# Kernel tuning notes

Hardware: AMD Instinct MI355X
Metric: run time of the kernel (lower is better)

## Reference

```python
import jax, jax.numpy as jnp
import numpy as np

NUM_HEADS = 16
ROPE_BASE = 10000.0


def _rope_cos_sin(seq_len, head_dim, dtype):
    # freqs for the half-dim; original caches cat(freqs, freqs) and then applies
    # the rotation per-half, which is equivalent to using the half-size tables.
    inv_freq = 1.0 / (ROPE_BASE ** (jnp.arange(0, head_dim, 2, dtype=jnp.float32) / head_dim))
    t = jnp.arange(seq_len, dtype=jnp.float32)
    freqs = jnp.einsum('i,j->ij', t, inv_freq)  # [S, hd/2]
    return jnp.cos(freqs).astype(dtype), jnp.sin(freqs).astype(dtype)


def _apply_rotary(x, cos, sin):
    # x: [B, H, S, hd]; cos/sin: [S, hd/2] broadcast over B, H
    half = x.shape[-1] // 2
    x1, x2 = x[..., :half], x[..., half:]
    return jnp.concatenate([x1 * cos - x2 * sin, x2 * cos + x1 * sin], axis=-1)


def setup_inputs() -> dict:
    key = jax.random.key(0)
    ks = jax.random.split(key, 5)
    D = 2048
    B, S = 2, 2048
    std = 1.0 / np.sqrt(D)
    return {
        'x': jax.random.normal(ks[0], (B, S, D), dtype=jnp.float32),
        'Wq': jax.random.normal(ks[1], (D, D), dtype=jnp.float32) * std,
        'Wk': jax.random.normal(ks[2], (D, D), dtype=jnp.float32) * std,
        'Wv': jax.random.normal(ks[3], (D, D), dtype=jnp.float32) * std,
        'Wo': jax.random.normal(ks[4], (D, D), dtype=jnp.float32) * std,
    }


def reference(x, Wq, Wk, Wv, Wo):
    B, S, D = x.shape
    H = NUM_HEADS
    hd = D // H
    scale = hd ** -0.5

    def proj(W):  # torch Linear: y = x @ W.T -> [B, H, S, hd]
        return (x @ W.T).reshape(B, S, H, hd).transpose(0, 2, 1, 3)

    q, k, v = proj(Wq), proj(Wk), proj(Wv)

    cos, sin = _rope_cos_sin(S, hd, x.dtype)
    q = _apply_rotary(q, cos, sin)
    k = _apply_rotary(k, cos, sin)

    scores = jnp.einsum('bhqd,bhkd->bhqk', q, k) * scale  # full O(S^2) scores
    attn = jax.nn.softmax(scores, axis=-1)
    out = jnp.einsum('bhqk,bhkd->bhqd', attn, v)
    out = out.transpose(0, 2, 1, 3).reshape(B, S, D)
    return out @ Wo.T
```

## Files before the change

kernel.cpp:

```cpp
#include <hip/hip_runtime.h>
#include <cstdint>

typedef __attribute__((ext_vector_type(8))) short bf16x8;
typedef __attribute__((ext_vector_type(4))) float f32x4;

__device__ inline unsigned short f2bf(float f) {
  uint32_t u = __float_as_uint(f);
  uint32_t lsb = (u >> 16) & 1u;
  u += 0x7fffu + lsb;
  return (unsigned short)(u >> 16);
}
__device__ inline float bf2f(unsigned short b) {
  return __uint_as_float(((uint32_t)b) << 16);
}

#define GLOAD16(gp, lp)                                                        \
  __builtin_amdgcn_global_load_lds(                                            \
      (const __attribute__((address_space(1))) void*)(gp),                     \
      (__attribute__((address_space(3))) void*)(lp), 16, 0, 0)

__global__ void cvt_f32_bf16(const float* __restrict__ in,
                             unsigned short* __restrict__ out, int n) {
  int i = (blockIdx.x * 256 + threadIdx.x) * 4;
  if (i >= n) return;
  float4 v = *(const float4*)(in + i);
  unsigned short o[4] = {f2bf(v.x), f2bf(v.y), f2bf(v.z), f2bf(v.w)};
  *(uint64_t*)(out + i) = *(const uint64_t*)o;
}

__global__ void rope_table_k(float* __restrict__ ctab, float* __restrict__ stab) {
  int i = blockIdx.x * 256 + threadIdx.x;
  int s = i >> 6, j = i & 63;
  float invf = expf(-(float)j * (9.210340371976184f / 64.0f));
  float ang = (float)s * invf;
  ctab[i] = cosf(ang);
  stab[i] = sinf(ang);
}

__global__ void rope_apply_k(unsigned short* __restrict__ qb,
                             unsigned short* __restrict__ kb,
                             const float* __restrict__ ctab,
                             const float* __restrict__ stab) {
  int row = blockIdx.x * 4 + (threadIdx.x >> 6);
  int t = threadIdx.x & 63;
  int s = row & 2047;
  int bh = (row >> 11) & 31;
  unsigned short* base = (row >> 16) ? kb : qb;
  unsigned short* p = base + ((size_t)bh * 2048 + s) * 128;
  float c = ctab[s * 64 + t], sn = stab[s * 64 + t];
  float x1 = bf2f(p[t]), x2 = bf2f(p[t + 64]);
  p[t] = f2bf(x1 * c - x2 * sn);
  p[t + 64] = f2bf(x2 * c + x1 * sn);
}

__global__ void transpose_v_k(const unsigned short* __restrict__ v,
                              unsigned short* __restrict__ vt) {
  __shared__ unsigned short tile[64][72];
  int bh = blockIdx.x, st = blockIdx.y, dt = blockIdx.z;
  const unsigned short* src = v + ((size_t)bh * 2048 + st * 64) * 128 + dt * 64;
  unsigned short* dst = vt + ((size_t)bh * 128 + dt * 64) * 2048 + st * 64;
  int t = threadIdx.x;
  int r = t >> 2, c0 = (t & 3) * 16;
  *(bf16x8*)&tile[r][c0] = *(const bf16x8*)(src + (size_t)r * 128 + c0);
  *(bf16x8*)&tile[r][c0 + 8] = *(const bf16x8*)(src + (size_t)r * 128 + c0 + 8);
  __syncthreads();
  unsigned short o[16];
#pragma unroll
  for (int i = 0; i < 16; i++) o[i] = tile[c0 + i][r];
  *(bf16x8*)(dst + (size_t)r * 2048 + c0) = *(const bf16x8*)&o[0];
  *(bf16x8*)(dst + (size_t)r * 2048 + c0 + 8) = *(const bf16x8*)&o[8];
}

template <int EPI>
__global__ __launch_bounds__(256, 2) void gemm_bt(
    const unsigned short* __restrict__ A, const unsigned short* __restrict__ Bm,
    float* __restrict__ Cf, unsigned short* __restrict__ q_out,
    unsigned short* __restrict__ k_out, unsigned short* __restrict__ v_out,
    int M, int N, int K) {
  __shared__ unsigned short sA[128 * 32];
  __shared__ unsigned short sB[128 * 32];
  const int t = threadIdx.x;
  const int w = t >> 6, l = t & 63;
  const int wr = w >> 1, wc = w & 1;
  const int bm = blockIdx.x * 128, bn = blockIdx.y * 128;
  const int lr = l & 15, lg = l >> 4;
  f32x4 acc[4][4] = {};

  const int srow = w * 16 + (l >> 2);
  const int sseg = (l & 3) * 8;
  const unsigned short* ga = A + (size_t)(bm + srow) * K + sseg;
  const unsigned short* gb = Bm + (size_t)(bn + srow) * K + sseg;
  unsigned short* lA = sA + w * 512 + l * 8;
  unsigned short* lB = sB + w * 512 + l * 8;

  for (int kt = 0; kt < K; kt += 32) {
    __syncthreads();
    GLOAD16(ga + kt, lA);
    GLOAD16(ga + kt + (size_t)64 * K, lA + 2048);
    GLOAD16(gb + kt, lB);
    GLOAD16(gb + kt + (size_t)64 * K, lB + 2048);
    __syncthreads();
    bf16x8 af[4], bfv[4];
#pragma unroll
    for (int m = 0; m < 4; m++)
      af[m] = *(const bf16x8*)(sA + (wr * 64 + m * 16 + lr) * 32 + lg * 8);
#pragma unroll
    for (int n = 0; n < 4; n++)
      bfv[n] = *(const bf16x8*)(sB + (wc * 64 + n * 16 + lr) * 32 + lg * 8);
#pragma unroll
    for (int m = 0; m < 4; m++)
#pragma unroll
      for (int n = 0; n < 4; n++)
        acc[m][n] = __builtin_amdgcn_mfma_f32_16x16x32_bf16(af[m], bfv[n],
                                                            acc[m][n], 0, 0, 0);
  }

#pragma unroll
  for (int m = 0; m < 4; m++) {
#pragma unroll
    for (int n = 0; n < 4; n++) {
      int gm0 = bm + wr * 64 + m * 16 + lg * 4;
      int gn = bn + wc * 64 + n * 16 + lr;
#pragma unroll
      for (int j = 0; j < 4; j++) {
        float v = acc[m][n][j];
        int gm = gm0 + j;
        if (EPI == 0) {
          Cf[(size_t)gm * N + gn] = v;
        } else {
          int which = gn >> 11, rem = gn & 2047;
          int h = rem >> 7, d = rem & 127;
          int b = gm >> 11, s = gm & 2047;
          unsigned short* dst = which == 0 ? q_out : (which == 1 ? k_out : v_out);
          dst[(((size_t)(b * 16 + h)) * 2048 + s) * 128 + d] = f2bf(v);
        }
      }
    }
  }
}

__global__ __launch_bounds__(256, 2) void attn_k(
    const unsigned short* __restrict__ Q, const unsigned short* __restrict__ K,
    const unsigned short* __restrict__ Vt, unsigned short* __restrict__ ctx) {
  __shared__ unsigned short sK[2][64 * 128];
  __shared__ unsigned short sV[2][128 * 64];
  __shared__ unsigned short sP[4][16 * 72];

  const int bh = blockIdx.x, qt = blockIdx.y;
  const int t = threadIdx.x;
  const int w = t >> 6, l = t & 63;
  const int lr = l & 15, lg = l >> 4;
  const int b = bh >> 4, h = bh & 15;
  const int q0 = qt * 64 + w * 16;
  const unsigned short* Qp = Q + ((size_t)bh * 2048 + q0) * 128;
  const unsigned short* Kbh = K + (size_t)bh * 2048 * 128;
  const unsigned short* Vbh = Vt + (size_t)bh * 128 * 2048;

  int gko[4], gvo[4];
#pragma unroll
  for (int i = 0; i < 4; i++) {
    int p = i * 256 + t;
    int rK = p >> 4, cK = p & 15;
    gko[i] = rK * 128 + ((cK ^ (rK & 7)) * 8);
    int rV = p >> 3, cV = p & 7;
    gvo[i] = rV * 2048 + ((cV ^ (rV & 7)) * 8);
  }

  bf16x8 qf[4];
#pragma unroll
  for (int ks = 0; ks < 4; ks++)
    qf[ks] = *(const bf16x8*)(Qp + lr * 128 + ks * 32 + lg * 8);

  f32x4 o[8];
#pragma unroll
  for (int i = 0; i < 8; i++) o[i] = (f32x4)0.0f;
  float m_r = -1e30f, l_r = 0.0f;
  const float kSc = 0.08838834764831845f * 1.4426950408889634f;
  char* pl = (char*)sP[w];

#define STAGE_KV(buf, kv)                                                      \
  do {                                                                         \
    _Pragma("unroll") for (int i = 0; i < 4; i++)                              \
        GLOAD16(Kbh + (size_t)(kv)*128 + gko[i],                               \
                sK[buf] + (i * 256 + t) * 8);                                  \
    _Pragma("unroll") for (int i = 0; i < 4; i++)                              \
        GLOAD16(Vbh + (size_t)(kv) + gvo[i], sV[buf] + (i * 256 + t) * 8);     \
  } while (0)

  STAGE_KV(0, 0);
  __syncthreads();

  for (int it = 0; it < 32; ++it) {
    const int cur = it & 1;
    if (it < 31) STAGE_KV(cur ^ 1, (it + 1) * 64);

    const char* kb = (const char*)sK[cur];
    const char* vbb = (const char*)sV[cur];

    f32x4 st[4];
#pragma unroll
    for (int mf = 0; mf < 4; mf++) {
      st[mf] = (f32x4)0.0f;
      const int rr = mf * 16 + lr;
      const int sw = (rr & 7) << 4;
#pragma unroll
      for (int ks = 0; ks < 4; ks++) {
        bf16x8 kf = *(const bf16x8*)(kb + rr * 256 + ((ks * 64 + lg * 16) ^ sw));
        st[mf] = __builtin_amdgcn_mfma_f32_16x16x32_bf16(kf, qf[ks], st[mf], 0, 0, 0);
      }
    }

    float sm[16];
    float tmax = -1e30f;
#pragma unroll
    for (int i = 0; i < 16; i++) {
      sm[i] = st[i >> 2][i & 3] * kSc;
      tmax = fmaxf(tmax, sm[i]);
    }
    tmax = fmaxf(tmax, __shfl_xor(tmax, 16));
    tmax = fmaxf(tmax, __shfl_xor(tmax, 32));
    float m_new = fmaxf(m_r, tmax);
    float fac = exp2f(m_r - m_new);
    float psum = 0.0f;
#pragma unroll
    for (int i = 0; i < 16; i++) {
      sm[i] = exp2f(sm[i] - m_new);
      psum += sm[i];
    }
    psum += __shfl_xor(psum, 16);
    psum += __shfl_xor(psum, 32);
    l_r = l_r * fac + psum;
    m_r = m_new;

#pragma unroll
    for (int mf = 0; mf < 4; mf++) {
      unsigned short pk[4];
#pragma unroll
      for (int j = 0; j < 4; j++) pk[j] = f2bf(sm[mf * 4 + j]);
      *(uint64_t*)(pl + lr * 144 + mf * 32 + lg * 8) = *(const uint64_t*)pk;
    }

    float fo[4];
#pragma unroll
    for (int j = 0; j < 4; j++) fo[j] = __shfl(fac, lg * 4 + j);
#pragma unroll
    for (int nf = 0; nf < 8; nf++)
#pragma unroll
      for (int j = 0; j < 4; j++) o[nf][j] *= fo[j];

    bf16x8 pa[2];
#pragma unroll
    for (int ks2 = 0; ks2 < 2; ks2++)
      pa[ks2] = *(const bf16x8*)(pl + lr * 144 + ks2 * 64 + lg * 16);
#pragma unroll
    for (int nf = 0; nf < 8; nf++) {
      const int rv = nf * 16 + lr;
      const int sw = (rv & 7) << 4;
#pragma unroll
      for (int ks2 = 0; ks2 < 2; ks2++) {
        bf16x8 vb = *(const bf16x8*)(vbb + rv * 128 + ((ks2 * 64 + lg * 16) ^ sw));
        o[nf] = __builtin_amdgcn_mfma_f32_16x16x32_bf16(pa[ks2], vb, o[nf], 0, 0, 0);
      }
    }
    __syncthreads();
  }

  float inv = 1.0f / l_r;
  float io[4];
#pragma unroll
  for (int j = 0; j < 4; j++) io[j] = __shfl(inv, lg * 4 + j);
#pragma unroll
  for (int nf = 0; nf < 8; nf++) {
#pragma unroll
    for (int j = 0; j < 4; j++) {
      int s = q0 + lg * 4 + j;
      ctx[((size_t)(b * 2048 + s)) * 2048 + h * 128 + nf * 16 + lr] =
          f2bf(o[nf][j] * io[j]);
    }
  }
}

extern "C" void kernel_launch(void* const* d_in, const int* in_sizes, int n_in,
                              void* d_out, int out_size, void* d_ws,
                              size_t ws_size, hipStream_t stream) {
  const float* x = (const float*)d_in[0];
  const float* Wq = (const float*)d_in[1];
  const float* Wk = (const float*)d_in[2];
  const float* Wv = (const float*)d_in[3];
  const float* Wo = (const float*)d_in[4];
  float* out = (float*)d_out;

  const size_t BS = 4096;
  const size_t D = 2048;

  char* p = (char*)d_ws;
  unsigned short* xb = (unsigned short*)p;   p += BS * D * 2;
  unsigned short* wqkv = (unsigned short*)p; p += 3 * D * D * 2;
  unsigned short* wo = (unsigned short*)p;   p += D * D * 2;
  unsigned short* qb = (unsigned short*)p;   p += BS * D * 2;
  unsigned short* kb = (unsigned short*)p;   p += BS * D * 2;
  unsigned short* vb = (unsigned short*)p;   p += BS * D * 2;
  float* ctab = (float*)p;                   p += 2048 * 64 * 4;
  float* stab = (float*)p;                   p += 2048 * 64 * 4;
  unsigned short* vt = wqkv;
  unsigned short* ctx = xb;

  cvt_f32_bf16<<<8388608 / 1024, 256, 0, stream>>>(x, xb, 8388608);
  cvt_f32_bf16<<<4194304 / 1024, 256, 0, stream>>>(Wq, wqkv, 4194304);
  cvt_f32_bf16<<<4194304 / 1024, 256, 0, stream>>>(Wk, wqkv + 4194304, 4194304);
  cvt_f32_bf16<<<4194304 / 1024, 256, 0, stream>>>(Wv, wqkv + 8388608, 4194304);
  cvt_f32_bf16<<<4194304 / 1024, 256, 0, stream>>>(Wo, wo, 4194304);
  rope_table_k<<<131072 / 256, 256, 0, stream>>>(ctab, stab);

  gemm_bt<1><<<dim3(32, 48), 256, 0, stream>>>(xb, wqkv, nullptr, qb, kb, vb,
                                               4096, 6144, 2048);
  rope_apply_k<<<32768, 256, 0, stream>>>(qb, kb, ctab, stab);
  transpose_v_k<<<dim3(32, 32, 2), 256, 0, stream>>>(vb, vt);
  attn_k<<<dim3(32, 32), 256, 0, stream>>>(qb, kb, vt, ctx);
  gemm_bt<0><<<dim3(32, 16), 256, 0, stream>>>(ctx, wo, out, nullptr, nullptr,
                                               nullptr, 4096, 2048, 2048);
}
```

Baseline: 356.5 us.

## Rewrite attention with 32x32 MFMA tiles, register-resident P and lazy rescale

The attention kernel moves from 16x16x32 to 32x32x16 bf16 MFMA, with each wave handling 32 query rows and each block 128. The probability tile is packed and exchanged between lane halves with shuffles instead of going through shared memory. The softmax scale is folded into Q during the RoPE pass, and the running-max rescale of the output is skipped unless the new max exceeds the old by more than 8 in log2 units. This cuts LDS traffic, per-iteration ALU work and K/V reloads per query, at the cost of more registers per thread and half as many blocks.

New measurement: 316.3 us. 11.3% less time.

```diff
diff --git a/kernel.cpp b/kernel.cpp
--- a/kernel.cpp
+++ b/kernel.cpp
@@ -3,6 +3,7 @@
 
 typedef __attribute__((ext_vector_type(8))) short bf16x8;
 typedef __attribute__((ext_vector_type(4))) float f32x4;
+typedef __attribute__((ext_vector_type(16))) float f32x16;
 
 __device__ inline unsigned short f2bf(float f) {
   uint32_t u = __float_as_uint(f);
@@ -12,6 +13,11 @@
 }
 __device__ inline float bf2f(unsigned short b) {
   return __uint_as_float(((uint32_t)b) << 16);
+}
+__device__ inline uint32_t cvt_pk_bf16(float lo, float hi) {
+  uint32_t r;
+  asm volatile("v_cvt_pk_bf16_f32 %0, %1, %2" : "=v"(r) : "v"(lo), "v"(hi));
+  return r;
 }
 
 #define GLOAD16(gp, lp)                                                        \
@@ -45,12 +51,14 @@
   int t = threadIdx.x & 63;
   int s = row & 2047;
   int bh = (row >> 11) & 31;
-  unsigned short* base = (row >> 16) ? kb : qb;
+  int isK = row >> 16;
+  unsigned short* base = isK ? kb : qb;
+  float qs = isK ? 1.0f : (0.08838834764831845f * 1.4426950408889634f);
   unsigned short* p = base + ((size_t)bh * 2048 + s) * 128;
   float c = ctab[s * 64 + t], sn = stab[s * 64 + t];
   float x1 = bf2f(p[t]), x2 = bf2f(p[t + 64]);
-  p[t] = f2bf(x1 * c - x2 * sn);
-  p[t + 64] = f2bf(x2 * c + x1 * sn);
+  p[t] = f2bf((x1 * c - x2 * sn) * qs);
+  p[t + 64] = f2bf((x2 * c + x1 * sn) * qs);
 }
 
 __global__ void transpose_v_k(const unsigned short* __restrict__ v,
@@ -144,14 +152,14 @@
     const unsigned short* __restrict__ Vt, unsigned short* __restrict__ ctx) {
   __shared__ unsigned short sK[2][64 * 128];
   __shared__ unsigned short sV[2][128 * 64];
-  __shared__ unsigned short sP[4][16 * 72];
-
-  const int bh = blockIdx.x, qt = blockIdx.y;
+
+  const int qt = blockIdx.x, bh = blockIdx.y;
   const int t = threadIdx.x;
   const int w = t >> 6, l = t & 63;
-  const int lr = l & 15, lg = l >> 4;
-  const int b = bh >> 4, h = bh & 15;
-  const int q0 = qt * 64 + w * 16;
+  const int lq = l & 31;
+  const int h5 = l >> 5;
+  const int b = bh >> 4, hh = bh & 15;
+  const int q0 = qt * 128 + w * 32;
   const unsigned short* Qp = Q + ((size_t)bh * 2048 + q0) * 128;
   const unsigned short* Kbh = K + (size_t)bh * 2048 * 128;
   const unsigned short* Vbh = Vt + (size_t)bh * 128 * 2048;
@@ -166,17 +174,15 @@
     gvo[i] = rV * 2048 + ((cV ^ (rV & 7)) * 8);
   }
 
-  bf16x8 qf[4];
-#pragma unroll
-  for (int ks = 0; ks < 4; ks++)
-    qf[ks] = *(const bf16x8*)(Qp + lr * 128 + ks * 32 + lg * 8);
-
-  f32x4 o[8];
-#pragma unroll
-  for (int i = 0; i < 8; i++) o[i] = (f32x4)0.0f;
+  bf16x8 qf[8];
+#pragma unroll
+  for (int st = 0; st < 8; st++)
+    qf[st] = *(const bf16x8*)(Qp + lq * 128 + st * 16 + h5 * 8);
+
+  f32x16 o[4];
+#pragma unroll
+  for (int db = 0; db < 4; db++) o[db] = (f32x16)0.0f;
   float m_r = -1e30f, l_r = 0.0f;
-  const float kSc = 0.08838834764831845f * 1.4426950408889634f;
-  char* pl = (char*)sP[w];
 
 #define STAGE_KV(buf, kv)                                                      \
   do {                                                                         \
@@ -194,88 +200,106 @@
     const int cur = it & 1;
     if (it < 31) STAGE_KV(cur ^ 1, (it + 1) * 64);
 
-    const char* kb = (const char*)sK[cur];
-    const char* vbb = (const char*)sV[cur];
-
-    f32x4 st[4];
-#pragma unroll
-    for (int mf = 0; mf < 4; mf++) {
-      st[mf] = (f32x4)0.0f;
-      const int rr = mf * 16 + lr;
-      const int sw = (rr & 7) << 4;
-#pragma unroll
-      for (int ks = 0; ks < 4; ks++) {
-        bf16x8 kf = *(const bf16x8*)(kb + rr * 256 + ((ks * 64 + lg * 16) ^ sw));
-        st[mf] = __builtin_amdgcn_mfma_f32_16x16x32_bf16(kf, qf[ks], st[mf], 0, 0, 0);
+    const char* kbuf = (const char*)sK[cur];
+    const char* vbuf = (const char*)sV[cur];
+
+    f32x16 s2[2];
+#pragma unroll
+    for (int kb2 = 0; kb2 < 2; kb2++) {
+      s2[kb2] = (f32x16)0.0f;
+      const int rr = kb2 * 32 + lq;
+      const int swz = (rr & 7) << 4;
+#pragma unroll
+      for (int st = 0; st < 8; st++) {
+        bf16x8 kf = *(const bf16x8*)(kbuf + rr * 256 + ((st * 32 + h5 * 16) ^ swz));
+        s2[kb2] = __builtin_amdgcn_mfma_f32_32x32x16_bf16(kf, qf[st], s2[kb2], 0, 0, 0);
       }
     }
 
-    float sm[16];
-    float tmax = -1e30f;
-#pragma unroll
-    for (int i = 0; i < 16; i++) {
-      sm[i] = st[i >> 2][i & 3] * kSc;
-      tmax = fmaxf(tmax, sm[i]);
-    }
-    tmax = fmaxf(tmax, __shfl_xor(tmax, 16));
+    float sm[32];
+#pragma unroll
+    for (int kb2 = 0; kb2 < 2; kb2++)
+#pragma unroll
+      for (int r = 0; r < 16; r++) sm[kb2 * 16 + r] = s2[kb2][r];
+
+    float tmax = sm[0];
+#pragma unroll
+    for (int i = 1; i < 32; i++) tmax = fmaxf(tmax, sm[i]);
     tmax = fmaxf(tmax, __shfl_xor(tmax, 32));
-    float m_new = fmaxf(m_r, tmax);
-    float fac = exp2f(m_r - m_new);
+
+    if (!__all(tmax <= m_r + 8.0f)) {
+      float m_new = fmaxf(m_r, tmax);
+      float fac = exp2f(m_r - m_new);
+      l_r *= fac;
+      float fo[16];
+#pragma unroll
+      for (int r = 0; r < 16; r++)
+        fo[r] = __shfl(fac, (r & 3) + 8 * (r >> 2) + 4 * h5);
+#pragma unroll
+      for (int db = 0; db < 4; db++)
+#pragma unroll
+        for (int r = 0; r < 16; r++) o[db][r] *= fo[r];
+      m_r = m_new;
+    }
+
     float psum = 0.0f;
 #pragma unroll
-    for (int i = 0; i < 16; i++) {
-      sm[i] = exp2f(sm[i] - m_new);
+    for (int i = 0; i < 32; i++) {
+      sm[i] = exp2f(sm[i] - m_r);
       psum += sm[i];
     }
-    psum += __shfl_xor(psum, 16);
     psum += __shfl_xor(psum, 32);
-    l_r = l_r * fac + psum;
-    m_r = m_new;
-
-#pragma unroll
-    for (int mf = 0; mf < 4; mf++) {
-      unsigned short pk[4];
-#pragma unroll
-      for (int j = 0; j < 4; j++) pk[j] = f2bf(sm[mf * 4 + j]);
-      *(uint64_t*)(pl + lr * 144 + mf * 32 + lg * 8) = *(const uint64_t*)pk;
-    }
-
-    float fo[4];
-#pragma unroll
-    for (int j = 0; j < 4; j++) fo[j] = __shfl(fac, lg * 4 + j);
-#pragma unroll
-    for (int nf = 0; nf < 8; nf++)
-#pragma unroll
-      for (int j = 0; j < 4; j++) o[nf][j] *= fo[j];
-
-    bf16x8 pa[2];
-#pragma unroll
-    for (int ks2 = 0; ks2 < 2; ks2++)
-      pa[ks2] = *(const bf16x8*)(pl + lr * 144 + ks2 * 64 + lg * 16);
-#pragma unroll
-    for (int nf = 0; nf < 8; nf++) {
-      const int rv = nf * 16 + lr;
-      const int sw = (rv & 7) << 4;
-#pragma unroll
-      for (int ks2 = 0; ks2 < 2; ks2++) {
-        bf16x8 vb = *(const bf16x8*)(vbb + rv * 128 + ((ks2 * 64 + lg * 16) ^ sw));
-        o[nf] = __builtin_amdgcn_mfma_f32_16x16x32_bf16(pa[ks2], vb, o[nf], 0, 0, 0);
+    l_r += psum;
+
+    uint32_t wAp[2][4], wBp[2][4];
+#pragma unroll
+    for (int kb2 = 0; kb2 < 2; kb2++)
+#pragma unroll
+      for (int rq = 0; rq < 4; rq++) {
+        wAp[kb2][rq] = cvt_pk_bf16(sm[kb2 * 16 + rq * 4 + 0], sm[kb2 * 16 + rq * 4 + 1]);
+        wBp[kb2][rq] = cvt_pk_bf16(sm[kb2 * 16 + rq * 4 + 2], sm[kb2 * 16 + rq * 4 + 3]);
       }
+
+#pragma unroll
+    for (int st = 0; st < 4; st++) {
+      const int kb2 = st >> 1, p2 = (st & 1) * 2;
+      uint32_t keepA = h5 ? wAp[kb2][p2 + 1] : wAp[kb2][p2];
+      uint32_t keepB = h5 ? wBp[kb2][p2 + 1] : wBp[kb2][p2];
+      uint32_t sendA = h5 ? wAp[kb2][p2] : wAp[kb2][p2 + 1];
+      uint32_t sendB = h5 ? wBp[kb2][p2] : wBp[kb2][p2 + 1];
+      uint32_t partA = __shfl_xor(sendA, 32);
+      uint32_t partB = __shfl_xor(sendB, 32);
+      union {
+        uint32_t u[4];
+        bf16x8 v;
+      } pu;
+      pu.u[0] = h5 ? partA : keepA;
+      pu.u[1] = h5 ? partB : keepB;
+      pu.u[2] = h5 ? keepA : partA;
+      pu.u[3] = h5 ? keepB : partB;
+#pragma unroll
+      for (int db = 0; db < 4; db++) {
+        const int rv = db * 32 + lq;
+        const int swz = (rv & 7) << 4;
+        bf16x8 vb = *(const bf16x8*)(vbuf + rv * 128 + ((st * 32 + h5 * 16) ^ swz));
+        o[db] = __builtin_amdgcn_mfma_f32_32x32x16_bf16(pu.v, vb, o[db], 0, 0, 0);
+      }
     }
     __syncthreads();
   }
 
   float inv = 1.0f / l_r;
-  float io[4];
-#pragma unroll
-  for (int j = 0; j < 4; j++) io[j] = __shfl(inv, lg * 4 + j);
-#pragma unroll
-  for (int nf = 0; nf < 8; nf++) {
-#pragma unroll
-    for (int j = 0; j < 4; j++) {
-      int s = q0 + lg * 4 + j;
-      ctx[((size_t)(b * 2048 + s)) * 2048 + h * 128 + nf * 16 + lr] =
-          f2bf(o[nf][j] * io[j]);
+  float io[16];
+#pragma unroll
+  for (int r = 0; r < 16; r++)
+    io[r] = __shfl(inv, (r & 3) + 8 * (r >> 2) + 4 * h5);
+#pragma unroll
+  for (int db = 0; db < 4; db++) {
+#pragma unroll
+    for (int r = 0; r < 16; r++) {
+      int s = q0 + (r & 3) + 8 * (r >> 2) + 4 * h5;
+      ctx[((size_t)(b * 2048 + s)) * 2048 + hh * 128 + db * 32 + lq] =
+          f2bf(o[db][r] * io[r]);
     }
   }
 }
@@ -316,7 +340,7 @@
                                                4096, 6144, 2048);
   rope_apply_k<<<32768, 256, 0, stream>>>(qb, kb, ctab, stab);
   transpose_v_k<<<dim3(32, 32, 2), 256, 0, stream>>>(vb, vt);
-  attn_k<<<dim3(32, 32), 256, 0, stream>>>(qb, kb, vt, ctx);
+  attn_k<<<dim3(16, 32), 256, 0, stream>>>(qb, kb, vt, ctx);
   gemm_bt<0><<<dim3(32, 16), 256, 0, stream>>>(ctx, wo, out, nullptr, nullptr,
                                                nullptr, 4096, 2048, 2048);
 }
```
